# Performance work log

Measured on AMD Instinct MI355X. Metric: run time of the kernel, lower is better.

## Reference

```python
import jax, jax.numpy as jnp
import numpy as np

C_IN = 34   # C*V = 2*17 channels after reshape
C_MID = 16
C_OUT = 3
N_LAYERS = 3
BN_EPS = 1e-5
NEG_SLOPE = 0.01


def setup_inputs() -> dict:
    key = jax.random.key(0)
    ks = jax.random.split(key, 16)
    B, C, T, V = 512, 2, 2048, 17
    s = 1.0 / np.sqrt(C_IN)
    inp = {
        "x": jax.random.normal(ks[0], (B, C, T, V), dtype=jnp.float32),
        # stacked per-layer 1x1-conv (linear) weights for Q/K/V of 3 attention layers
        "wq": jax.random.normal(ks[1], (N_LAYERS, C_IN, C_IN), dtype=jnp.float32) * s,
        "bq": jax.random.normal(ks[2], (N_LAYERS, C_IN), dtype=jnp.float32) * 0.02,
        "wk": jax.random.normal(ks[3], (N_LAYERS, C_IN, C_IN), dtype=jnp.float32) * s,
        "bk": jax.random.normal(ks[4], (N_LAYERS, C_IN), dtype=jnp.float32) * 0.02,
        "wv": jax.random.normal(ks[5], (N_LAYERS, C_IN, C_IN), dtype=jnp.float32) * s,
        "bv": jax.random.normal(ks[6], (N_LAYERS, C_IN), dtype=jnp.float32) * 0.02,
        # head: conv1 -> BN -> LeakyReLU -> conv2
        "w1": jax.random.normal(ks[7], (C_MID, C_IN), dtype=jnp.float32) * s,
        "b1": jax.random.normal(ks[8], (C_MID,), dtype=jnp.float32) * 0.02,
        "gamma": jnp.ones((C_MID,), dtype=jnp.float32),
        "beta": jnp.zeros((C_MID,), dtype=jnp.float32),
        "mean": jax.random.normal(ks[9], (C_MID,), dtype=jnp.float32) * 0.1,
        "var": jax.random.uniform(ks[10], (C_MID,), dtype=jnp.float32, minval=0.5, maxval=1.5),
        "w2": jax.random.normal(ks[11], (C_OUT, C_MID), dtype=jnp.float32) * (1.0 / np.sqrt(C_MID)),
        "b2": jax.random.normal(ks[12], (C_OUT,), dtype=jnp.float32) * 0.02,
    }
    return inp


def _conv1x1(w, b, h):
    # 1x1 Conv1d == linear over channel dim: (O,C) x (B,C,T) -> (B,O,T)
    return jnp.einsum('oc,bct->bot', w, h) + b[:, None]


def reference(x, wq, bq, wk, bk, wv, bv, w1, b1, gamma, beta, mean, var, w2, b2):
    B, C, T, V = x.shape
    h = x.transpose(0, 1, 3, 2).reshape(B, C * V, T)  # (B, 34, T)
    scale = 1.0 / (T ** 0.5)  # K.size(-1) ** 0.5 in the original
    for i in range(N_LAYERS):
        Q = _conv1x1(wq[i], bq[i], h)
        K = _conv1x1(wk[i], bk[i], h)
        Vv = _conv1x1(wv[i], bv[i], h)
        scores = jnp.einsum('bct,bdt->bcd', Q, K) * scale  # (B, 34, 34) channel attention
        attn = jax.nn.softmax(scores, axis=-1)
        h = jnp.einsum('bcd,bdt->bct', attn, Vv)
    y = _conv1x1(w1, b1, h)                               # (B, 16, T)
    inv = gamma / jnp.sqrt(var + BN_EPS)                  # inference-mode BatchNorm1d
    y = (y - mean[:, None]) * inv[:, None] + beta[:, None]
    y = jnp.where(y > 0, y, NEG_SLOPE * y)                # LeakyReLU
    return _conv1x1(w2, b2, y)                            # (B, 3, T)
```

## Files before the change

kernel.cpp:

```cpp
#include <hip/hip_runtime.h>

#define CV   34
#define TTOT 2048
#define NB   512
#define XB   69632
#define XC   34816

#define RB_STRIDE 576

typedef __attribute__((ext_vector_type(8))) short v8s;
typedef __attribute__((ext_vector_type(4))) float v4f;

__device__ __forceinline__ unsigned short f2bf(float f) {
    unsigned int u = __float_as_uint(f);
    u = u + 0x7FFFu + ((u >> 16) & 1u);
    return (unsigned short)(u >> 16);
}
__device__ __forceinline__ float bf2f(unsigned short s) {
    return __uint_as_float(((unsigned int)s) << 16);
}

__device__ __forceinline__ unsigned int cvtpk_bf16(float a, float b) {
    unsigned int r;
    asm("v_cvt_pk_bf16_f32 %0, %1, %2" : "=v"(r) : "v"(a), "v"(b));
    return r;
}

__device__ __forceinline__ void split8(const float (&f)[8], v8s* hi, v8s* lo) {
    union { unsigned int u[4]; v8s s; } H, L;
#pragma unroll
    for (int p = 0; p < 4; ++p) {
        float a = f[2 * p], b = f[2 * p + 1];
        unsigned int h = cvtpk_bf16(a, b);
        float ra = a - __uint_as_float(h << 16);
        float rb = b - __uint_as_float(h & 0xFFFF0000u);
        L.u[p] = cvtpk_bf16(ra, rb);
        H.u[p] = h;
    }
    *hi = H.s;
    *lo = L.s;
}

__device__ __forceinline__ void stage_chunk(const float* __restrict__ xb, int t0,
                                            float* rawbuf, int w, int lane) {
#pragma unroll
    for (int i = 0; i < 5; ++i) {
        int idx = i * 4 + w;
        if (idx < 17) {
            int fl = idx * 256 + lane * 4;
            int co = (fl >= 2176) ? 1 : 0;
            const float* g = xb + t0 * 17 + fl + co * 32640;
            __builtin_amdgcn_global_load_lds(
                (const __attribute__((address_space(1))) void*)g,
                (__attribute__((address_space(3))) void*)(rawbuf + idx * 256),
                16, 0, 0);
        }
    }
}

#define RST 44
#define RSZ (36 * RST)
#define R_G0 0
#define R_At (1 * RSZ)
#define R_Aq (2 * RSZ)
#define R_Ak (3 * RSZ)
#define R_Av (4 * RSZ)
#define R_S1 (5 * RSZ)
#define R_Sc (6 * RSZ)
#define R_Wx (7 * RSZ)
#define SMF  (8 * RSZ)

__device__ __forceinline__ void ldfrag8(const float* p, v8s* hi, v8s* lo) {
    float f[8];
    *(float4*)&f[0] = *(const float4*)p;
    *(float4*)&f[4] = *(const float4*)(p + 4);
    split8(f, hi, lo);
}

__device__ __forceinline__ void ldfrag4(const float* p, int quad, v8s* hi, v8s* lo) {
    union { unsigned int u[4]; v8s s; } H, L;
#pragma unroll
    for (int i = 0; i < 4; ++i) { H.u[i] = 0; L.u[i] = 0; }
    if (quad == 0) {
        float4 f = *(const float4*)p;
        unsigned int h0 = cvtpk_bf16(f.x, f.y);
        unsigned int h1 = cvtpk_bf16(f.z, f.w);
        float r0 = f.x - __uint_as_float(h0 << 16);
        float r1 = f.y - __uint_as_float(h0 & 0xFFFF0000u);
        float r2 = f.z - __uint_as_float(h1 << 16);
        float r3 = f.w - __uint_as_float(h1 & 0xFFFF0000u);
        H.u[0] = h0; H.u[1] = h1;
        L.u[0] = cvtpk_bf16(r0, r1);
        L.u[1] = cvtpk_bf16(r2, r3);
    }
    *hi = H.s;
    *lo = L.s;
}

__device__ __forceinline__ void mfma_mm3(float* __restrict__ SMD, int Lo, int Ro,
                                         int Do, int wave, int lane, bool transD) {
    if (wave >= 3) return;
    const int lc = lane & 15, quad = lane >> 4;
    const int tm = wave;
    int ra = tm * 16 + lc; ra = ra < 36 ? ra : 35;
    const float* pa = SMD + Lo + ra * RST;
    v8s Ah0, Al0, Ah1, Al1;
    ldfrag8(pa + quad * 8, &Ah0, &Al0);
    ldfrag4(pa + 32, quad, &Ah1, &Al1);
#pragma unroll
    for (int tn = 0; tn < 3; ++tn) {
        int rb = tn * 16 + lc; rb = rb < 36 ? rb : 35;
        const float* pb = SMD + Ro + rb * RST;
        v8s Bh0, Bl0, Bh1, Bl1;
        ldfrag8(pb + quad * 8, &Bh0, &Bl0);
        ldfrag4(pb + 32, quad, &Bh1, &Bl1);
        v4f acc = {0.f, 0.f, 0.f, 0.f};
        acc = __builtin_amdgcn_mfma_f32_16x16x32_bf16(Ah0, Bh0, acc, 0, 0, 0);
        acc = __builtin_amdgcn_mfma_f32_16x16x32_bf16(Ah0, Bl0, acc, 0, 0, 0);
        acc = __builtin_amdgcn_mfma_f32_16x16x32_bf16(Al0, Bh0, acc, 0, 0, 0);
        acc = __builtin_amdgcn_mfma_f32_16x16x32_bf16(Ah1, Bh1, acc, 0, 0, 0);
        acc = __builtin_amdgcn_mfma_f32_16x16x32_bf16(Ah1, Bl1, acc, 0, 0, 0);
        acc = __builtin_amdgcn_mfma_f32_16x16x32_bf16(Al1, Bh1, acc, 0, 0, 0);
        if (!transD) {
            int gcol = tn * 16 + lc;
            if (gcol < 36) {
#pragma unroll
                for (int i = 0; i < 4; ++i) {
                    int grow = tm * 16 + quad * 4 + i;
                    if (grow < 36) SMD[Do + grow * RST + gcol] = acc[i];
                }
            }
        } else {
            int trow = tn * 16 + lc;
            int tcol = tm * 16 + quad * 4;
            if (trow < 36 && tcol < 36)
                *(v4f*)&SMD[Do + trow * RST + tcol] = acc;
        }
    }
}

__global__ __launch_bounds__(256) void k_fused(
    const float* __restrict__ x,
    const float* __restrict__ wq, const float* __restrict__ bq,
    const float* __restrict__ wk, const float* __restrict__ bk,
    const float* __restrict__ wv, const float* __restrict__ bv,
    const float* __restrict__ w1, const float* __restrict__ b1,
    const float* __restrict__ gamma, const float* __restrict__ beta,
    const float* __restrict__ mean, const float* __restrict__ var,
    float* __restrict__ ws) {
    __shared__ __align__(16) float SMD[SMF];
    const int tid  = threadIdx.x;
    const int wave = tid >> 6;
    const int l    = tid & 63;
    const int b    = blockIdx.x;
    const int row16 = l & 15;
    const int quad  = l >> 4;
    const float* xb = x + (size_t)b * XB;

    float* raw0 = SMD + R_Aq;
    float* raw1 = SMD + R_Aq + 4352;

    int offc[3];
#pragma unroll
    for (int r = 0; r < 3; ++r) {
        int c = r * 16 + row16;
        if (c > 33) c = 33;
        offc[r] = (c >= 17) ? (2159 + c) : c;
    }
    const int koff = wave * 32 + quad * 8;

    v4f accG[3][3];
    v4f accS[3];
    {
        v4f vz = {0.f, 0.f, 0.f, 0.f};
#pragma unroll
        for (int r = 0; r < 3; ++r) {
            accS[r] = vz;
#pragma unroll
            for (int c = 0; c < 3; ++c) accG[r][c] = vz;
        }
    }
    v8s ones;
#pragma unroll
    for (int i = 0; i < 8; ++i) ones[i] = (short)0x3F80;

    stage_chunk(xb, 0, raw0, wave, l);
    __syncthreads();

    for (int ch = 0; ch < 16; ++ch) {
        float* cur = (ch & 1) ? raw1 : raw0;
        float* nxt = (ch & 1) ? raw0 : raw1;
        if (ch < 15) stage_chunk(xb, (ch + 1) * 128, nxt, wave, l);

        const float* rb = cur + koff * 17;
        v8s fh[3], fl4[3];
#pragma unroll
        for (int r = 0; r < 3; ++r) {
            const float* p = rb + offc[r];
            float f[8];
#pragma unroll
            for (int e = 0; e < 8; ++e) f[e] = p[e * 17];
            split8(f, &fh[r], &fl4[r]);
        }
#pragma unroll
        for (int r = 0; r < 3; ++r) {
#pragma unroll
            for (int c = 0; c < 3; ++c) {
                accG[r][c] = __builtin_amdgcn_mfma_f32_16x16x32_bf16(fh[r],  fh[c],  accG[r][c], 0, 0, 0);
                accG[r][c] = __builtin_amdgcn_mfma_f32_16x16x32_bf16(fh[r],  fl4[c], accG[r][c], 0, 0, 0);
                accG[r][c] = __builtin_amdgcn_mfma_f32_16x16x32_bf16(fl4[r], fh[c],  accG[r][c], 0, 0, 0);
            }
            accS[r] = __builtin_amdgcn_mfma_f32_16x16x32_bf16(fh[r],  ones, accS[r], 0, 0, 0);
            accS[r] = __builtin_amdgcn_mfma_f32_16x16x32_bf16(fl4[r], ones, accS[r], 0, 0, 0);
        }
        __syncthreads();
    }

    {
        float* gp = SMD + R_At + wave * RSZ;
#pragma unroll
        for (int r = 0; r < 3; ++r) {
#pragma unroll
            for (int c = 0; c < 3; ++c) {
#pragma unroll
                for (int i = 0; i < 4; ++i) {
                    int m = r * 16 + quad * 4 + i;
                    int n = c * 16 + row16;
                    if (m < 34 && n < 34) gp[m * RST + n] = accG[r][c][i];
                }
            }
            if (row16 == 0) {
#pragma unroll
                for (int i = 0; i < 4; ++i) {
                    int m = r * 16 + quad * 4 + i;
                    if (m < 34) gp[34 * RST + m] = accS[r][i];
                }
            }
        }
    }
    __syncthreads();
    float gred[5];
    int   gm[5], gn[5];
#pragma unroll
    for (int k = 0; k < 5; ++k) {
        int idx = tid + k * 256;
        if (idx < 1156) {
            int m = idx / 34, n = idx - m * 34;
            gm[k] = m; gn[k] = n;
            gred[k] = SMD[R_At + m * RST + n] + SMD[R_Aq + m * RST + n] +
                      SMD[R_Ak + m * RST + n] + SMD[R_Av + m * RST + n];
        } else { gm[k] = -1; gn[k] = 0; gred[k] = 0.f; }
    }
    float s0red = 0.f;
    if (tid < 34)
        s0red = SMD[R_At + 34 * RST + tid] + SMD[R_Aq + 34 * RST + tid] +
                SMD[R_Ak + 34 * RST + tid] + SMD[R_Av + 34 * RST + tid];
    __syncthreads();
    {
        const float4 z = make_float4(0.f, 0.f, 0.f, 0.f);
        for (int i = tid * 4; i < SMF; i += 1024) *(float4*)(SMD + i) = z;
    }
    __syncthreads();
#pragma unroll
    for (int k = 0; k < 5; ++k)
        if (gm[k] >= 0) SMD[R_G0 + gm[k] * RST + gn[k]] = gred[k];
    for (int idx = tid; idx < 1156; idx += 256) {
        int m = idx / 34, n = idx - m * 34;
        SMD[R_Aq + m * RST + n] = wq[idx];
        SMD[R_Ak + m * RST + n] = wk[idx];
        SMD[R_Av + n * RST + m] = wv[idx];
    }
    if (tid < 34) {
        SMD[R_G0 + 34 * RST + tid] = s0red;
        SMD[R_G0 + tid * RST + 34] = s0red;
        SMD[R_Aq + tid * RST + 34] = bq[tid];
        SMD[R_Ak + tid * RST + 34] = bk[tid];
        SMD[R_Av + 34 * RST + tid] = bv[tid];
    }
    if (tid == 0) SMD[R_G0 + 34 * RST + 34] = 2048.0f;
    __syncthreads();

    for (int lyr = 0; lyr < 3; ++lyr) {
        if (lyr > 0) {
            const float* wql = wq + lyr * 1156;
            const float* wkl = wk + lyr * 1156;
            const float* wvl = wv + lyr * 1156;
            for (int idx = tid; idx < 1156; idx += 256) {
                int m = idx / 34, n = idx - m * 34;
                SMD[R_S1 + m * RST + n] = wql[idx];
                SMD[R_Sc + m * RST + n] = wkl[idx];
                SMD[R_Wx + m * RST + n] = wvl[idx];
            }
            __syncthreads();
            mfma_mm3(SMD, R_S1, R_At, R_Aq, wave, l, false);
            mfma_mm3(SMD, R_Sc, R_At, R_Ak, wave, l, false);
            mfma_mm3(SMD, R_Wx, R_At, R_Av, wave, l, true);
            __syncthreads();
            if (tid < 34) {
                SMD[R_Aq + tid * RST + 34] += bq[lyr * 34 + tid];
                SMD[R_Ak + tid * RST + 34] += bk[lyr * 34 + tid];
                SMD[R_Av + 34 * RST + tid] += bv[lyr * 34 + tid];
            }
            __syncthreads();
        }
        mfma_mm3(SMD, R_Aq, R_G0, R_S1, wave, l, false);
        __syncthreads();
        mfma_mm3(SMD, R_S1, R_Ak, R_Sc, wave, l, false);
        __syncthreads();
        if (tid < 34) {
            float f[36];
#pragma unroll
            for (int e0 = 0; e0 < 36; e0 += 4)
                *(float4*)&f[e0] = *(const float4*)&SMD[R_Sc + tid * RST + e0];
            const float scale = 0.022097086912079608f;
            float mx = -1e30f;
#pragma unroll
            for (int d = 0; d < 34; ++d) { f[d] *= scale; mx = fmaxf(mx, f[d]); }
            float sum = 0.f;
#pragma unroll
            for (int d = 0; d < 34; ++d) { float e = __expf(f[d] - mx); f[d] = e; sum += e; }
            float rs = 1.0f / sum;
#pragma unroll
            for (int d = 0; d < 34; ++d) f[d] *= rs;
            f[34] = 0.f; f[35] = 0.f;
#pragma unroll
            for (int e0 = 0; e0 < 36; e0 += 4)
                *(float4*)&SMD[R_Sc + tid * RST + e0] = *(const float4*)&f[e0];
        } else if (tid >= 64 && tid < 82) {
            int u = tid - 64;
            int row = 34 + u / 9, c4 = (u - (u / 9) * 9) * 4;
            *(float4*)&SMD[R_Sc + row * RST + c4] = make_float4(0.f, 0.f, 0.f, 0.f);
        }
        __syncthreads();
        mfma_mm3(SMD, R_Av, R_Sc, R_At, wave, l, false);
        __syncthreads();
    }

    for (int idx = tid; idx < 544; idx += 256) {
        int m = idx / 34, n = idx - m * 34;
        SMD[R_Sc + m * RST + n] = w1[idx];
    }
    __syncthreads();
    mfma_mm3(SMD, R_Sc, R_At, R_S1, wave, l, false);
    __syncthreads();
    float* wb = ws + (size_t)b * RB_STRIDE;
    if (tid < 16) {
        float iv = gamma[tid] * rsqrtf(var[tid] + 1e-5f);
        float cyraw = SMD[R_S1 + tid * RST + 34] + b1[tid];
        wb[512 + tid] = (cyraw - mean[tid]) * iv + beta[tid];
        wb[528 + tid] = SMD[R_S1 + tid * RST + 32] * iv;
        wb[544 + tid] = SMD[R_S1 + tid * RST + 33] * iv;
    }
    unsigned short* wp = (unsigned short*)wb;
    for (int i = tid; i < 512; i += 256) {
        int o = i >> 5, c = i & 31;
        float iv = gamma[o] * rsqrtf(var[o] + 1e-5f);
        float vv = SMD[R_S1 + o * RST + c] * iv;
        unsigned short hb = f2bf(vv);
        wp[i] = hb;
        wp[512 + i] = f2bf(vv - bf2f(hb));
    }
}

__global__ __launch_bounds__(256, 4) void k_out(const float* __restrict__ x,
                                                const float* __restrict__ w2,
                                                const float* __restrict__ b2,
                                                const float* __restrict__ ws,
                                                float* __restrict__ out) {
    __shared__ __align__(16) float raw[2][4352];

    const int tid  = threadIdx.x;
    const int b    = blockIdx.x >> 3;
    const int seg  = (blockIdx.x & 7) * 256;
    const int l    = tid & 63;
    const int w    = tid >> 6;
    const int quad = l >> 4;
    const int col  = l & 15;

    const float* wb = ws + (size_t)b * RB_STRIDE;
    const unsigned short* wp = (const unsigned short*)wb;
    v8s aH = *(const v8s*)&wp[col * 32 + quad * 8];
    v8s aL = *(const v8s*)&wp[512 + col * 32 + quad * 8];
    float cyr[4], w2r[3][4], wy32r[4], wy33r[4];
#pragma unroll
    for (int i = 0; i < 4; ++i) {
        int o = quad * 4 + i;
        cyr[i]   = wb[512 + o];
        wy32r[i] = wb[528 + o];
        wy33r[i] = wb[544 + o];
#pragma unroll
        for (int p = 0; p < 3; ++p) w2r[p][i] = w2[p * 16 + o];
    }
    float b2r[3] = {b2[0], b2[1], b2[2]};
    const float* xb = x + (size_t)b * XB;

    int offq[8];
#pragma unroll
    for (int e = 0; e < 8; ++e) {
        int c = quad * 8 + e;
        offq[e] = (c >= 17) ? (2159 + c) : c;
    }

    stage_chunk(xb, seg, raw[0], w, l);
    __syncthreads();

    for (int ch = 0; ch < 2; ++ch) {
        if (ch == 0) stage_chunk(xb, seg + 128, raw[1], w, l);
        for (int tt = w; tt < 8; tt += 4) {
            const int tl = tt * 16 + col;
            const float* rbt = raw[ch] + tl * 17;
            float f[8];
#pragma unroll
            for (int e = 0; e < 8; ++e) f[e] = rbt[offq[e]];
            v8s bH, bL;
            split8(f, &bH, &bL);
            v4f acc = {0.f, 0.f, 0.f, 0.f};
            acc = __builtin_amdgcn_mfma_f32_16x16x32_bf16(aH, bH, acc, 0, 0, 0);
            acc = __builtin_amdgcn_mfma_f32_16x16x32_bf16(aH, bL, acc, 0, 0, 0);
            acc = __builtin_amdgcn_mfma_f32_16x16x32_bf16(aL, bH, acc, 0, 0, 0);
            float h32 = rbt[2191];
            float h33 = rbt[2192];
            float op[3] = {0, 0, 0};
#pragma unroll
            for (int i = 0; i < 4; ++i) {
                float y = acc[i] + cyr[i] + wy32r[i] * h32 + wy33r[i] * h33;
                float z = (y > 0.f) ? y : 0.01f * y;
#pragma unroll
                for (int p = 0; p < 3; ++p) op[p] += w2r[p][i] * z;
            }
#pragma unroll
            for (int p = 0; p < 3; ++p) {
                op[p] += __shfl_xor(op[p], 16);
                op[p] += __shfl_xor(op[p], 32);
            }
            if (l < 16) {
                int tg = seg + ch * 128 + tt * 16 + l;
#pragma unroll
                for (int p = 0; p < 3; ++p)
                    out[((size_t)b * 3 + p) * 2048 + tg] = op[p] + b2r[p];
            }
        }
        __syncthreads();
    }
}

extern "C" void kernel_launch(void* const* d_in, const int* in_sizes, int n_in,
                              void* d_out, int out_size, void* d_ws, size_t ws_size,
                              hipStream_t stream) {
    const float* x     = (const float*)d_in[0];
    const float* wq    = (const float*)d_in[1];
    const float* bq    = (const float*)d_in[2];
    const float* wk    = (const float*)d_in[3];
    const float* bk    = (const float*)d_in[4];
    const float* wv    = (const float*)d_in[5];
    const float* bv    = (const float*)d_in[6];
    const float* w1    = (const float*)d_in[7];
    const float* b1    = (const float*)d_in[8];
    const float* gamma = (const float*)d_in[9];
    const float* beta  = (const float*)d_in[10];
    const float* mean  = (const float*)d_in[11];
    const float* var   = (const float*)d_in[12];
    const float* w2    = (const float*)d_in[13];
    const float* b2    = (const float*)d_in[14];
    float* ws  = (float*)d_ws;
    float* out = (float*)d_out;

    k_fused<<<dim3(512), dim3(256), 0, stream>>>(x, wq, bq, wk, bk, wv, bv,
                                                 w1, b1, gamma, beta, mean, var, ws);
    k_out<<<dim3(4096), dim3(256), 0, stream>>>(x, w2, b2, ws, out);
}
```

Measured before the change: 277.2 us.

## Double k_fused block to 512 threads with two chunk-streaming wave groups

k_fused now runs 8 waves per block instead of 4. The waves form two groups that stream alternating 128-column chunks of x, each into its own double buffer, and their Gram partials are summed across 8 slots. The small 36x36 matrix products are now split into 16x16 tiles handed out round-robin over all 8 waves, where before only 3 waves did them. This is meant to add memory-level parallelism and latency hiding to the Gram pass and to spread the per-layer tile work. In exchange it uses more shared memory and registers per block, which may lower occupancy.

```diff
diff --git a/kernel.cpp b/kernel.cpp
--- a/kernel.cpp
+++ b/kernel.cpp
@@ -69,6 +69,7 @@
 #define R_Sc (6 * RSZ)
 #define R_Wx (7 * RSZ)
 #define SMF  (8 * RSZ)
+#define STF  17408
 
 __device__ __forceinline__ void ldfrag8(const float* p, v8s* hi, v8s* lo) {
     float f[8];
@@ -97,49 +98,45 @@
     *lo = L.s;
 }
 
-__device__ __forceinline__ void mfma_mm3(float* __restrict__ SMD, int Lo, int Ro,
-                                         int Do, int wave, int lane, bool transD) {
-    if (wave >= 3) return;
+__device__ __forceinline__ void tile_mm(float* __restrict__ SMD, int Lo, int Ro,
+                                        int Do, int tm, int tn, int lane,
+                                        bool transD) {
     const int lc = lane & 15, quad = lane >> 4;
-    const int tm = wave;
     int ra = tm * 16 + lc; ra = ra < 36 ? ra : 35;
     const float* pa = SMD + Lo + ra * RST;
     v8s Ah0, Al0, Ah1, Al1;
     ldfrag8(pa + quad * 8, &Ah0, &Al0);
     ldfrag4(pa + 32, quad, &Ah1, &Al1);
-#pragma unroll
-    for (int tn = 0; tn < 3; ++tn) {
-        int rb = tn * 16 + lc; rb = rb < 36 ? rb : 35;
-        const float* pb = SMD + Ro + rb * RST;
-        v8s Bh0, Bl0, Bh1, Bl1;
-        ldfrag8(pb + quad * 8, &Bh0, &Bl0);
-        ldfrag4(pb + 32, quad, &Bh1, &Bl1);
-        v4f acc = {0.f, 0.f, 0.f, 0.f};
-        acc = __builtin_amdgcn_mfma_f32_16x16x32_bf16(Ah0, Bh0, acc, 0, 0, 0);
-        acc = __builtin_amdgcn_mfma_f32_16x16x32_bf16(Ah0, Bl0, acc, 0, 0, 0);
-        acc = __builtin_amdgcn_mfma_f32_16x16x32_bf16(Al0, Bh0, acc, 0, 0, 0);
-        acc = __builtin_amdgcn_mfma_f32_16x16x32_bf16(Ah1, Bh1, acc, 0, 0, 0);
-        acc = __builtin_amdgcn_mfma_f32_16x16x32_bf16(Ah1, Bl1, acc, 0, 0, 0);
-        acc = __builtin_amdgcn_mfma_f32_16x16x32_bf16(Al1, Bh1, acc, 0, 0, 0);
-        if (!transD) {
-            int gcol = tn * 16 + lc;
-            if (gcol < 36) {
-#pragma unroll
-                for (int i = 0; i < 4; ++i) {
-                    int grow = tm * 16 + quad * 4 + i;
-                    if (grow < 36) SMD[Do + grow * RST + gcol] = acc[i];
-                }
-            }
-        } else {
-            int trow = tn * 16 + lc;
-            int tcol = tm * 16 + quad * 4;
-            if (trow < 36 && tcol < 36)
-                *(v4f*)&SMD[Do + trow * RST + tcol] = acc;
-        }
-    }
-}
-
-__global__ __launch_bounds__(256) void k_fused(
+    int rb = tn * 16 + lc; rb = rb < 36 ? rb : 35;
+    const float* pb = SMD + Ro + rb * RST;
+    v8s Bh0, Bl0, Bh1, Bl1;
+    ldfrag8(pb + quad * 8, &Bh0, &Bl0);
+    ldfrag4(pb + 32, quad, &Bh1, &Bl1);
+    v4f acc = {0.f, 0.f, 0.f, 0.f};
+    acc = __builtin_amdgcn_mfma_f32_16x16x32_bf16(Ah0, Bh0, acc, 0, 0, 0);
+    acc = __builtin_amdgcn_mfma_f32_16x16x32_bf16(Ah0, Bl0, acc, 0, 0, 0);
+    acc = __builtin_amdgcn_mfma_f32_16x16x32_bf16(Al0, Bh0, acc, 0, 0, 0);
+    acc = __builtin_amdgcn_mfma_f32_16x16x32_bf16(Ah1, Bh1, acc, 0, 0, 0);
+    acc = __builtin_amdgcn_mfma_f32_16x16x32_bf16(Ah1, Bl1, acc, 0, 0, 0);
+    acc = __builtin_amdgcn_mfma_f32_16x16x32_bf16(Al1, Bh1, acc, 0, 0, 0);
+    if (!transD) {
+        int gcol = tn * 16 + lc;
+        if (gcol < 36) {
+#pragma unroll
+            for (int i = 0; i < 4; ++i) {
+                int grow = tm * 16 + quad * 4 + i;
+                if (grow < 36) SMD[Do + grow * RST + gcol] = acc[i];
+            }
+        }
+    } else {
+        int trow = tn * 16 + lc;
+        int tcol = tm * 16 + quad * 4;
+        if (trow < 36 && tcol < 36)
+            *(v4f*)&SMD[Do + trow * RST + tcol] = acc;
+    }
+}
+
+__global__ __launch_bounds__(512) void k_fused(
     const float* __restrict__ x,
     const float* __restrict__ wq, const float* __restrict__ bq,
     const float* __restrict__ wk, const float* __restrict__ bk,
@@ -148,18 +145,17 @@
     const float* __restrict__ gamma, const float* __restrict__ beta,
     const float* __restrict__ mean, const float* __restrict__ var,
     float* __restrict__ ws) {
-    __shared__ __align__(16) float SMD[SMF];
+    __shared__ __align__(16) float SMD[STF];
     const int tid  = threadIdx.x;
     const int wave = tid >> 6;
+    const int wsub = wave & 3;
+    const int g    = wave >> 2;
     const int l    = tid & 63;
     const int b    = blockIdx.x;
     const int row16 = l & 15;
     const int quad  = l >> 4;
     const float* xb = x + (size_t)b * XB;
 
-    float* raw0 = SMD + R_Aq;
-    float* raw1 = SMD + R_Aq + 4352;
-
     int offc[3];
 #pragma unroll
     for (int r = 0; r < 3; ++r) {
@@ -167,7 +163,7 @@
         if (c > 33) c = 33;
         offc[r] = (c >= 17) ? (2159 + c) : c;
     }
-    const int koff = wave * 32 + quad * 8;
+    const int koff = wsub * 32 + quad * 8;
 
     v4f accG[3][3];
     v4f accS[3];
@@ -184,13 +180,17 @@
 #pragma unroll
     for (int i = 0; i < 8; ++i) ones[i] = (short)0x3F80;
 
-    stage_chunk(xb, 0, raw0, wave, l);
-    __syncthreads();
-
-    for (int ch = 0; ch < 16; ++ch) {
-        float* cur = (ch & 1) ? raw1 : raw0;
-        float* nxt = (ch & 1) ? raw0 : raw1;
-        if (ch < 15) stage_chunk(xb, (ch + 1) * 128, nxt, wave, l);
+    float* buf0 = SMD + (g * 2 + 0) * 4352;
+    float* buf1 = SMD + (g * 2 + 1) * 4352;
+
+    stage_chunk(xb, g * 128, buf0, wsub, l);
+    __syncthreads();
+
+    for (int i = 0; i < 8; ++i) {
+        const int myChunk = 2 * i + g;
+        float* cur = (i & 1) ? buf1 : buf0;
+        float* nxt = (i & 1) ? buf0 : buf1;
+        if (i < 7) stage_chunk(xb, (myChunk + 2) * 128, nxt, wsub, l);
 
         const float* rb = cur + koff * 17;
         v8s fh[3], fl4[3];
@@ -217,7 +217,7 @@
     }
 
     {
-        float* gp = SMD + R_At + wave * RSZ;
+        float* gp = SMD + wave * RSZ;
 #pragma unroll
         for (int r = 0; r < 3; ++r) {
 #pragma unroll
@@ -239,32 +239,35 @@
         }
     }
     __syncthreads();
-    float gred[5];
-    int   gm[5], gn[5];
-#pragma unroll
-    for (int k = 0; k < 5; ++k) {
-        int idx = tid + k * 256;
+    float gred[3];
+    int   gm[3], gn[3];
+#pragma unroll
+    for (int k = 0; k < 3; ++k) {
+        int idx = tid + k * 512;
         if (idx < 1156) {
             int m = idx / 34, n = idx - m * 34;
             gm[k] = m; gn[k] = n;
-            gred[k] = SMD[R_At + m * RST + n] + SMD[R_Aq + m * RST + n] +
-                      SMD[R_Ak + m * RST + n] + SMD[R_Av + m * RST + n];
+            float s = 0.f;
+#pragma unroll
+            for (int r = 0; r < 8; ++r) s += SMD[r * RSZ + m * RST + n];
+            gred[k] = s;
         } else { gm[k] = -1; gn[k] = 0; gred[k] = 0.f; }
     }
     float s0red = 0.f;
-    if (tid < 34)
-        s0red = SMD[R_At + 34 * RST + tid] + SMD[R_Aq + 34 * RST + tid] +
-                SMD[R_Ak + 34 * RST + tid] + SMD[R_Av + 34 * RST + tid];
+    if (tid < 34) {
+#pragma unroll
+        for (int r = 0; r < 8; ++r) s0red += SMD[r * RSZ + 34 * RST + tid];
+    }
     __syncthreads();
     {
         const float4 z = make_float4(0.f, 0.f, 0.f, 0.f);
-        for (int i = tid * 4; i < SMF; i += 1024) *(float4*)(SMD + i) = z;
-    }
-    __syncthreads();
-#pragma unroll
-    for (int k = 0; k < 5; ++k)
+        for (int i = tid * 4; i < SMF; i += 2048) *(float4*)(SMD + i) = z;
+    }
+    __syncthreads();
+#pragma unroll
+    for (int k = 0; k < 3; ++k)
         if (gm[k] >= 0) SMD[R_G0 + gm[k] * RST + gn[k]] = gred[k];
-    for (int idx = tid; idx < 1156; idx += 256) {
+    for (int idx = tid; idx < 1156; idx += 512) {
         int m = idx / 34, n = idx - m * 34;
         SMD[R_Aq + m * RST + n] = wq[idx];
         SMD[R_Ak + m * RST + n] = wk[idx];
@@ -285,16 +288,20 @@
             const float* wql = wq + lyr * 1156;
             const float* wkl = wk + lyr * 1156;
             const float* wvl = wv + lyr * 1156;
-            for (int idx = tid; idx < 1156; idx += 256) {
+            for (int idx = tid; idx < 1156; idx += 512) {
                 int m = idx / 34, n = idx - m * 34;
                 SMD[R_S1 + m * RST + n] = wql[idx];
                 SMD[R_Sc + m * RST + n] = wkl[idx];
                 SMD[R_Wx + m * RST + n] = wvl[idx];
             }
             __syncthreads();
-            mfma_mm3(SMD, R_S1, R_At, R_Aq, wave, l, false);
-            mfma_mm3(SMD, R_Sc, R_At, R_Ak, wave, l, false);
-            mfma_mm3(SMD, R_Wx, R_At, R_Av, wave, l, true);
+            for (int t = wave; t < 27; t += 8) {
+                int mmI = t / 9, tile = t - mmI * 9;
+                int tm = tile / 3, tn = tile - tm * 3;
+                int Lo = (mmI == 0) ? R_S1 : (mmI == 1) ? R_Sc : R_Wx;
+                int Do = (mmI == 0) ? R_Aq : (mmI == 1) ? R_Ak : R_Av;
+                tile_mm(SMD, Lo, R_At, Do, tm, tn, l, mmI == 2);
+            }
             __syncthreads();
             if (tid < 34) {
                 SMD[R_Aq + tid * RST + 34] += bq[lyr * 34 + tid];
@@ -303,9 +310,15 @@
             }
             __syncthreads();
         }
-        mfma_mm3(SMD, R_Aq, R_G0, R_S1, wave, l, false);
-        __syncthreads();
-        mfma_mm3(SMD, R_S1, R_Ak, R_Sc, wave, l, false);
+        for (int t = wave; t < 9; t += 8) {
+            int tm = t / 3, tn = t - tm * 3;
+            tile_mm(SMD, R_Aq, R_G0, R_S1, tm, tn, l, false);
+        }
+        __syncthreads();
+        for (int t = wave; t < 9; t += 8) {
+            int tm = t / 3, tn = t - tm * 3;
+            tile_mm(SMD, R_S1, R_Ak, R_Sc, tm, tn, l, false);
+        }
         __syncthreads();
         if (tid < 34) {
             float f[36];
@@ -332,16 +345,22 @@
             *(float4*)&SMD[R_Sc + row * RST + c4] = make_float4(0.f, 0.f, 0.f, 0.f);
         }
         __syncthreads();
-        mfma_mm3(SMD, R_Av, R_Sc, R_At, wave, l, false);
-        __syncthreads();
-    }
-
-    for (int idx = tid; idx < 544; idx += 256) {
+        for (int t = wave; t < 9; t += 8) {
+            int tm = t / 3, tn = t - tm * 3;
+            tile_mm(SMD, R_Av, R_Sc, R_At, tm, tn, l, false);
+        }
+        __syncthreads();
+    }
+
+    for (int idx = tid; idx < 544; idx += 512) {
         int m = idx / 34, n = idx - m * 34;
         SMD[R_Sc + m * RST + n] = w1[idx];
     }
     __syncthreads();
-    mfma_mm3(SMD, R_Sc, R_At, R_S1, wave, l, false);
+    for (int t = wave; t < 9; t += 8) {
+        int tm = t / 3, tn = t - tm * 3;
+        tile_mm(SMD, R_Sc, R_At, R_S1, tm, tn, l, false);
+    }
     __syncthreads();
     float* wb = ws + (size_t)b * RB_STRIDE;
     if (tid < 16) {
@@ -352,7 +371,7 @@
         wb[544 + tid] = SMD[R_S1 + tid * RST + 33] * iv;
     }
     unsigned short* wp = (unsigned short*)wb;
-    for (int i = tid; i < 512; i += 256) {
+    for (int i = tid; i < 512; i += 512) {
         int o = i >> 5, c = i & 31;
         float iv = gamma[o] * rsqrtf(var[o] + 1e-5f);
         float vv = SMD[R_S1 + o * RST + c] * iv;
@@ -465,7 +484,7 @@
     float* ws  = (float*)d_ws;
     float* out = (float*)d_out;
 
-    k_fused<<<dim3(512), dim3(256), 0, stream>>>(x, wq, bq, wk, bk, wv, bv,
+    k_fused<<<dim3(512), dim3(512), 0, stream>>>(x, wq, bq, wk, bk, wv, bv,
                                                  w1, b1, gamma, beta, mean, var, ws);
     k_out<<<dim3(4096), dim3(256), 0, stream>>>(x, w2, b2, ws, out);
 }
```

Result: no change. 278.6 us (+0.5%).
